# Kernel optimization log

Hardware: AMD Instinct MI355X
Metric: run time of the kernel (lower is better)

The kernel has to match this reference:

```python
import jax, jax.numpy as jnp
import numpy as np

B, N, H, D = 2, 2048, 8, 64  # batch, seq, heads, out_channels (per-head, incl. time dim)
E = H * 64                   # embed dim = num_heads * in_channels
C = 1.0                      # manifold curvature c
EPS = 1e-8


def setup_inputs() -> dict:
    key = jax.random.key(0)
    ks = jax.random.split(key, 8)
    d_out = H * (D - 1)
    inp = {
        "query_input": jax.random.normal(ks[0], (B, N, E), dtype=jnp.float32),
        "source_input": jax.random.normal(ks[1], (B, N, E), dtype=jnp.float32),
        "Wq_w": jax.random.normal(ks[2], (d_out, E), dtype=jnp.float32) * 0.02,
        "Wq_b": jnp.zeros((d_out,), dtype=jnp.float32),
        "Wk_w": jax.random.normal(ks[3], (d_out, E), dtype=jnp.float32) * 0.02,
        "Wk_b": jnp.zeros((d_out,), dtype=jnp.float32),
        "Wv_w": jax.random.normal(ks[4], (d_out, E), dtype=jnp.float32) * 0.02,
        "Wv_b": jnp.zeros((d_out,), dtype=jnp.float32),
        "scale": jnp.array([np.sqrt(H * D)], dtype=jnp.float32),
        "bias": jnp.zeros((), dtype=jnp.float32),
    }
    return inp


def _lift(x_space):
    # project space coords onto hyperboloid: prepend time = sqrt(||x||^2 + c)
    t = jnp.sqrt(jnp.sum(x_space * x_space, axis=-1, keepdims=True) + C)
    return jnp.concatenate([t, x_space], axis=-1)  # [..., D]


def _centroid(ave):
    # Lorentzian centroid normalization: sqrt(c) * ave / sqrt(|<ave,ave>_L|)
    inner = jnp.sum(ave * ave, axis=-1, keepdims=True) - 2.0 * ave[..., :1] ** 2
    denom = jnp.sqrt(jnp.maximum(jnp.abs(inner), EPS))
    return jnp.sqrt(C) * ave / denom


def reference(query_input, source_input, Wq_w, Wq_b, Wk_w, Wk_b, Wv_w, Wv_b, scale, bias):
    def heads(x, W, b):
        return (x @ W.T + b).reshape(B, N, H, D - 1)

    q = _lift(heads(query_input, Wq_w, Wq_b))   # [B,N,H,D]
    k = _lift(heads(source_input, Wk_w, Wk_b))  # [B,N,H,D]
    v = _lift(heads(source_input, Wv_w, Wv_b))  # [B,N,H,D]

    # Lorentzian inner product: negate time component of q
    sign = jnp.concatenate([-jnp.ones((1,), q.dtype), jnp.ones((D - 1,), q.dtype)])
    att = 2.0 * C + 2.0 * jnp.einsum('bnhd,bmhd->bhnm', q * sign, k)  # [B,H,N,N]
    att = att / scale[0] + bias
    w = jax.nn.softmax(att, axis=-1)

    ave = jnp.einsum('bhnm,bmhd->bnhd', w, v)   # weighted sum of values
    out = _centroid(ave)                         # per-head hyperbolic centroid [B,N,H,D]
    out = _centroid(jnp.mean(out, axis=2))       # centroid across heads -> [B,N,D]
    return out
```

## Files before the change

kernel.cpp:

```cpp
#include <hip/hip_runtime.h>
#include <math.h>
#include <stdint.h>

#define BB   2
#define NN   2048
#define HH   8
#define DD   64
#define EE   512
#define DM1  63

typedef _Float16 half8  __attribute__((ext_vector_type(8)));
typedef __fp16   fp16x2 __attribute__((ext_vector_type(2)));
typedef float    floatx4 __attribute__((ext_vector_type(4)));

__device__ __forceinline__ uint32_t pkh2(float a, float b) {
    union { fp16x2 h; uint32_t u; } uu;
    uu.h = __builtin_amdgcn_cvt_pkrtz(a, b);
    return uu.u;
}

__global__ __launch_bounds__(256, 3) void qkv_mfma(
    const float* __restrict__ Xq, const float* __restrict__ Xs,
    const float* __restrict__ Wq, const float* __restrict__ Wk,
    const float* __restrict__ Wv,
    const float* __restrict__ Wqb, const float* __restrict__ Wkb,
    const float* __restrict__ Wvb, const float* __restrict__ scale_p,
    _Float16* __restrict__ q16, _Float16* __restrict__ k16,
    _Float16* __restrict__ vT16)
{
    const int mtb = blockIdx.x;
    const int hp  = blockIdx.y;
    const int mat = blockIdx.z;
    const int t    = threadIdx.x;
    const int w    = t >> 6;
    const int lane = t & 63;
    const int l15  = lane & 15;
    const int quad = lane >> 4;

    __shared__ alignas(16) char smem[27648];
    __shared__ float psum[64][4];
    _Float16 (*Xsh)[72]  = (_Float16(*)[72])smem;
    _Float16 (*Wsh)[72]  = (_Float16(*)[72])(smem + 9216);
    _Float16 (*Osh)[136] = (_Float16(*)[136])(smem + 9216);
    _Float16 (*OshT)[72] = (_Float16(*)[72])(smem + 9216);

    const float* X    = (mat == 0) ? Xq : Xs;
    const float* W    = (mat == 0) ? Wq : (mat == 1 ? Wk : Wv);
    const float* bias = (mat == 0) ? Wqb : (mat == 1 ? Wkb : Wvb);
    const int tok0 = mtb * 64;

    floatx4 acc[4][2];
#pragma unroll
    for (int mt = 0; mt < 4; mt++)
#pragma unroll
        for (int nt = 0; nt < 2; nt++) acc[mt][nt] = (floatx4){0.f,0.f,0.f,0.f};

    float4 pxa[2], pxb[2], pwa[4], pwb[4];
#pragma unroll
    for (int ls = 0; ls < 2; ls++) {
        int g = t + 256 * ls, r = g >> 3, c = g & 7;
        const float* p = X + (size_t)(tok0 + r) * EE + c * 8;
        pxa[ls] = *(const float4*)p;
        pxb[ls] = *(const float4*)(p + 4);
    }
#pragma unroll
    for (int ls = 0; ls < 4; ls++) {
        int g = t + 256 * ls, r = g >> 3, c = g & 7;
        int head = r >> 6, j = r & 63;
        pwa[ls] = make_float4(0.f,0.f,0.f,0.f);
        pwb[ls] = make_float4(0.f,0.f,0.f,0.f);
        if (j < DM1) {
            const float* p = W + (size_t)((hp * 2 + head) * DM1 + j) * EE + c * 8;
            pwa[ls] = *(const float4*)p;
            pwb[ls] = *(const float4*)(p + 4);
        }
    }

    for (int it = 0; it < 8; it++) {
        __syncthreads();
#pragma unroll
        for (int ls = 0; ls < 2; ls++) {
            int g = t + 256 * ls, r = g >> 3, c = g & 7;
            uint4 h;
            h.x = pkh2(pxa[ls].x, pxa[ls].y); h.y = pkh2(pxa[ls].z, pxa[ls].w);
            h.z = pkh2(pxb[ls].x, pxb[ls].y); h.w = pkh2(pxb[ls].z, pxb[ls].w);
            *(uint4*)&Xsh[r][c * 8] = h;
        }
#pragma unroll
        for (int ls = 0; ls < 4; ls++) {
            int g = t + 256 * ls, r = g >> 3, c = g & 7;
            uint4 h;
            h.x = pkh2(pwa[ls].x, pwa[ls].y); h.y = pkh2(pwa[ls].z, pwa[ls].w);
            h.z = pkh2(pwb[ls].x, pwb[ls].y); h.w = pkh2(pwb[ls].z, pwb[ls].w);
            *(uint4*)&Wsh[r][c * 8] = h;
        }
        __syncthreads();
        if (it + 1 < 8) {
            int ek = (it + 1) * 64;
#pragma unroll
            for (int ls = 0; ls < 2; ls++) {
                int g = t + 256 * ls, r = g >> 3, c = g & 7;
                const float* p = X + (size_t)(tok0 + r) * EE + ek + c * 8;
                pxa[ls] = *(const float4*)p;
                pxb[ls] = *(const float4*)(p + 4);
            }
#pragma unroll
            for (int ls = 0; ls < 4; ls++) {
                int g = t + 256 * ls, r = g >> 3, c = g & 7;
                int head = r >> 6, j = r & 63;
                if (j < DM1) {
                    const float* p = W + (size_t)((hp * 2 + head) * DM1 + j) * EE + ek + c * 8;
                    pwa[ls] = *(const float4*)p;
                    pwb[ls] = *(const float4*)(p + 4);
                }
            }
        }
#pragma unroll
        for (int kk = 0; kk < 2; kk++) {
            half8 a[4];
#pragma unroll
            for (int mt = 0; mt < 4; mt++)
                a[mt] = *(const half8*)&Xsh[mt * 16 + l15][kk * 32 + quad * 8];
#pragma unroll
            for (int nt = 0; nt < 2; nt++) {
                half8 bfr = *(const half8*)&Wsh[w * 32 + nt * 16 + l15][kk * 32 + quad * 8];
#pragma unroll
                for (int mt = 0; mt < 4; mt++)
                    acc[mt][nt] = __builtin_amdgcn_mfma_f32_16x16x32_f16(
                        a[mt], bfr, acc[mt][nt], 0, 0, 0);
            }
        }
    }
    __syncthreads();

    const float st   = 2.0f / scale_p[0];
    const float fmul = (mat == 0) ? st : 1.0f;

    float vals[4][2][4];
    float sqp[4][4];
#pragma unroll
    for (int mt = 0; mt < 4; mt++)
#pragma unroll
        for (int r = 0; r < 4; r++) sqp[mt][r] = 0.f;

#pragma unroll
    for (int mt = 0; mt < 4; mt++)
#pragma unroll
        for (int nt = 0; nt < 2; nt++) {
            int col = w * 32 + nt * 16 + l15;
            int head = col >> 6, j = col & 63;
            float bb = (j < DM1) ? bias[(hp * 2 + head) * DM1 + j] : 0.f;
#pragma unroll
            for (int r = 0; r < 4; r++) {
                float vv = acc[mt][nt][r] + bb;
                if (j >= DM1) vv = 0.f;
                vals[mt][nt][r] = vv;
                sqp[mt][r] += vv * vv;
            }
        }
#pragma unroll
    for (int mt = 0; mt < 4; mt++)
#pragma unroll
        for (int r = 0; r < 4; r++) {
            float s = sqp[mt][r];
            s += __shfl_xor(s, 1, 64); s += __shfl_xor(s, 2, 64);
            s += __shfl_xor(s, 4, 64); s += __shfl_xor(s, 8, 64);
            if (l15 == 0) psum[mt * 16 + quad * 4 + r][w] = s;
        }

    if (mat < 2) {
#pragma unroll
        for (int mt = 0; mt < 4; mt++)
#pragma unroll
            for (int nt = 0; nt < 2; nt++) {
                int col = w * 32 + nt * 16 + l15;
                int head = col >> 6, j = col & 63;
                if (j < DM1) {
                    int dc = head * 64 + 1 + j;
#pragma unroll
                    for (int r = 0; r < 4; r++)
                        Osh[mt * 16 + quad * 4 + r][dc] = (_Float16)(vals[mt][nt][r] * fmul);
                }
            }
    } else {
#pragma unroll
        for (int mt = 0; mt < 4; mt++)
#pragma unroll
            for (int nt = 0; nt < 2; nt++) {
                int col = w * 32 + nt * 16 + l15;
                uint2 pu;
                pu.x = pkh2(vals[mt][nt][0], vals[mt][nt][1]);
                pu.y = pkh2(vals[mt][nt][2], vals[mt][nt][3]);
                *(uint2*)&OshT[col][mt * 16 + quad * 4] = pu;
            }
    }
    __syncthreads();
    if (t < 64) {
        float tsA = sqrtf(psum[t][0] + psum[t][1] + 1.0f);
        float tsB = sqrtf(psum[t][2] + psum[t][3] + 1.0f);
        if (mat < 2) {
            float tm = (mat == 0) ? -st : 1.0f;
            Osh[t][0]  = (_Float16)(tsA * tm);
            Osh[t][64] = (_Float16)(tsB * tm);
        } else {
            OshT[63][t]  = (_Float16)tsA;
            OshT[127][t] = (_Float16)tsB;
        }
    }
    __syncthreads();

    const int bI = tok0 >> 11, n0 = tok0 & 2047;
    if (mat < 2) {
        _Float16* O = (mat == 0) ? q16 : k16;
#pragma unroll
        for (int ls = 0; ls < 4; ls++) {
            int s = t + 256 * ls, r = s >> 4, c = s & 15, head = c >> 3;
            size_t bh = (size_t)(bI * HH + hp * 2 + head);
            *(uint4*)&O[(bh * NN + n0 + r) * DD + (c & 7) * 8] = *(const uint4*)&Osh[r][c * 8];
        }
    } else {
#pragma unroll
        for (int ls = 0; ls < 4; ls++) {
            int s = t + 256 * ls, df = s >> 3, c = s & 7;
            int head = df >> 6, d = df & 63;
            int rr = head * 64 + ((d + 63) & 63);
            size_t bh = (size_t)(bI * HH + hp * 2 + head);
            *(uint4*)&vT16[(bh * DD + d) * NN + n0 + c * 8] = *(const uint4*)&OshT[rr][c * 8];
        }
    }
}

__global__ __launch_bounds__(256, 3) void lorentz_attn_v8(
    const _Float16* __restrict__ q16, const _Float16* __restrict__ k16,
    const _Float16* __restrict__ vT16,
    _Float16* __restrict__ Odh, float* __restrict__ Ors)
{
    const int qt = blockIdx.x;
    const int bh = blockIdx.y;
    const int ks = blockIdx.z;
    const int t    = threadIdx.x;
    const int w    = t >> 6;
    const int lane = t & 63;
    const int l15  = lane & 15;
    const int quad = lane >> 4;

    __shared__ alignas(16) char smem[36864];
    _Float16 (*Ks)[72]  = (_Float16(*)[72])smem;
    _Float16 (*VTs)[72] = (_Float16(*)[72])(smem + 9216);
    _Float16 (*Psw)[72] = (_Float16(*)[72])(smem + 18432 + w * 4608);

    const _Float16* kb = k16  + (size_t)bh * NN * DD;
    const _Float16* vb = vT16 + (size_t)bh * DD * NN;
    const int kt0 = ks * 8;

    half8 qb[2][2];
#pragma unroll
    for (int mt = 0; mt < 2; mt++) {
        const _Float16* qrow = q16 +
            ((size_t)bh * NN + qt * 128 + w * 32 + mt * 16 + l15) * DD;
        qb[mt][0] = *(const half8*)&qrow[quad * 8];
        qb[mt][1] = *(const half8*)&qrow[32 + quad * 8];
    }

    half8 vones;
#pragma unroll
    for (int i = 0; i < 8; i++) vones[i] = (_Float16)1.0f;

    uint4 pk[2], pv[2];
#pragma unroll
    for (int ls = 0; ls < 2; ls++) {
        int s = t + 256 * ls, r = s >> 3, c = s & 7;
        pk[ls] = *(const uint4*)&kb[((size_t)kt0 * 64 + r) * DD + c * 8];
        pv[ls] = *(const uint4*)&vb[(size_t)r * NN + kt0 * 64 + c * 8];
    }
#pragma unroll
    for (int ls = 0; ls < 2; ls++) {
        int s = t + 256 * ls, r = s >> 3, c = s & 7;
        *(uint4*)&Ks[r][c * 8]  = pk[ls];
        *(uint4*)&VTs[r][c * 8] = pv[ls];
    }
    __syncthreads();

    floatx4 oacc[2][5];
#pragma unroll
    for (int mt = 0; mt < 2; mt++)
#pragma unroll
        for (int nt = 0; nt < 5; nt++) oacc[mt][nt] = (floatx4){0.f,0.f,0.f,0.f};

    for (int i = 0; i < 8; i++) {
        const int kt = kt0 + i;
        if (i + 1 < 8) {
#pragma unroll
            for (int ls = 0; ls < 2; ls++) {
                int s = t + 256 * ls, r = s >> 3, c = s & 7;
                pk[ls] = *(const uint4*)&kb[((size_t)(kt + 1) * 64 + r) * DD + c * 8];
                pv[ls] = *(const uint4*)&vb[(size_t)r * NN + (kt + 1) * 64 + c * 8];
            }
        }
        floatx4 sacc[4][2];
#pragma unroll
        for (int nt = 0; nt < 4; nt++)
#pragma unroll
            for (int mt = 0; mt < 2; mt++) sacc[nt][mt] = (floatx4){0.f,0.f,0.f,0.f};
#pragma unroll
        for (int kk = 0; kk < 2; kk++)
#pragma unroll
            for (int nt = 0; nt < 4; nt++) {
                half8 kf = *(const half8*)&Ks[nt * 16 + l15][kk * 32 + quad * 8];
#pragma unroll
                for (int mt = 0; mt < 2; mt++)
                    sacc[nt][mt] = __builtin_amdgcn_mfma_f32_16x16x32_f16(
                        kf, qb[mt][kk], sacc[nt][mt], 0, 0, 0);
            }
#pragma unroll
        for (int nt = 0; nt < 4; nt++)
#pragma unroll
            for (int mt = 0; mt < 2; mt++) {
                uint2 pu;
                pu.x = pkh2(__expf(sacc[nt][mt][0]), __expf(sacc[nt][mt][1]));
                pu.y = pkh2(__expf(sacc[nt][mt][2]), __expf(sacc[nt][mt][3]));
                *(uint2*)&Psw[mt * 16 + l15][nt * 16 + quad * 4] = pu;
            }
        half8 pa[2][2];
#pragma unroll
        for (int mt = 0; mt < 2; mt++) {
            pa[mt][0] = *(const half8*)&Psw[mt * 16 + l15][quad * 8];
            pa[mt][1] = *(const half8*)&Psw[mt * 16 + l15][32 + quad * 8];
        }
#pragma unroll
        for (int kk = 0; kk < 2; kk++) {
#pragma unroll
            for (int nt = 0; nt < 4; nt++) {
                half8 vf = *(const half8*)&VTs[nt * 16 + l15][kk * 32 + quad * 8];
#pragma unroll
                for (int mt = 0; mt < 2; mt++)
                    oacc[mt][nt] = __builtin_amdgcn_mfma_f32_16x16x32_f16(
                        pa[mt][kk], vf, oacc[mt][nt], 0, 0, 0);
            }
#pragma unroll
            for (int mt = 0; mt < 2; mt++)
                oacc[mt][4] = __builtin_amdgcn_mfma_f32_16x16x32_f16(
                    pa[mt][kk], vones, oacc[mt][4], 0, 0, 0);
        }
        __syncthreads();
        if (i + 1 < 8) {
#pragma unroll
            for (int ls = 0; ls < 2; ls++) {
                int s = t + 256 * ls, r = s >> 3, c = s & 7;
                *(uint4*)&Ks[r][c * 8]  = pk[ls];
                *(uint4*)&VTs[r][c * 8] = pv[ls];
            }
            __syncthreads();
        }
    }

    const size_t obase = (((size_t)ks * 16 + bh) * NN + qt * 128 + w * 32);
    float* slab = (float*)Psw;
#pragma unroll
    for (int mt = 0; mt < 2; mt++) {
#pragma unroll
        for (int nt = 0; nt < 4; nt++)
#pragma unroll
            for (int r = 0; r < 4; r++)
                slab[(quad * 4 + r) * 68 + nt * 16 + l15] = oacc[mt][nt][r];
#pragma unroll
        for (int i = 0; i < 4; i++) {
            int s = lane + 64 * i, row = s >> 4, c4 = (s & 15) * 4;
            float4 v = *(const float4*)&slab[row * 68 + c4];
            uint2 pu;
            pu.x = pkh2(v.x, v.y);
            pu.y = pkh2(v.z, v.w);
            *(uint2*)&Odh[(obase + mt * 16 + row) * 64 + c4] = pu;
        }
        if (l15 == 0) {
#pragma unroll
            for (int r = 0; r < 4; r++)
                Ors[obase + mt * 16 + quad * 4 + r] = oacc[mt][4][r];
        }
    }
}

__global__ __launch_bounds__(256) void merge_centroid(
    const _Float16* __restrict__ Odh, const float* __restrict__ Ors,
    float* __restrict__ out)
{
    const int t    = threadIdx.x;
    const int tok  = blockIdx.x * 4 + (t >> 6);
    const int lane = t & 63;
    const int b = tok >> 11;
    const int n = tok & 2047;

    float m = 0.f;
#pragma unroll
    for (int h = 0; h < HH; h++) {
        const size_t bh = (size_t)(b * HH + h);
        float o = 0.f, rs = 0.f;
#pragma unroll
        for (int ksp = 0; ksp < 4; ksp++) {
            const size_t row = ((size_t)ksp * 16 + bh) * NN + n;
            o  += (float)Odh[row * 64 + lane];
            rs += Ors[row];
        }
        float a  = o / rs;
        float ssq = a * a;
#pragma unroll
        for (int off = 32; off > 0; off >>= 1)
            ssq += __shfl_xor(ssq, off, 64);
        float a0 = __shfl(a, 0, 64);
        float inner = ssq - 2.0f * a0 * a0;
        float f = rsqrtf(fmaxf(fabsf(inner), 1e-8f));
        m += a * f;
    }
    m *= 0.125f;

    float sq = m * m;
#pragma unroll
    for (int off = 32; off > 0; off >>= 1)
        sq += __shfl_xor(sq, off, 64);
    float m0 = __shfl(m, 0, 64);
    float inner = sq - 2.0f * m0 * m0;
    float f = rsqrtf(fmaxf(fabsf(inner), 1e-8f));
    out[(size_t)tok * DD + lane] = m * f;
}

extern "C" void kernel_launch(void* const* d_in, const int* in_sizes, int n_in,
                              void* d_out, int out_size, void* d_ws, size_t ws_size,
                              hipStream_t stream)
{
    const float* Xq  = (const float*)d_in[0];
    const float* Xs  = (const float*)d_in[1];
    const float* Wq  = (const float*)d_in[2];
    const float* Wqb = (const float*)d_in[3];
    const float* Wk  = (const float*)d_in[4];
    const float* Wkb = (const float*)d_in[5];
    const float* Wv  = (const float*)d_in[6];
    const float* Wvb = (const float*)d_in[7];
    const float* sc  = (const float*)d_in[8];
    float* out = (float*)d_out;

    const size_t QSZ = (size_t)BB * HH * NN * DD;
    _Float16* q16  = (_Float16*)d_ws;
    _Float16* k16  = q16 + QSZ;
    _Float16* vT16 = k16 + QSZ;
    _Float16* Odh  = vT16 + QSZ;
    float* Ors = (float*)(Odh + (size_t)4 * 16 * NN * 64);

    qkv_mfma<<<dim3(64, 4, 3), 256, 0, stream>>>(Xq, Xs, Wq, Wk, Wv,
                                                 Wqb, Wkb, Wvb, sc,
                                                 q16, k16, vT16);
    lorentz_attn_v8<<<dim3(16, 16, 4), 256, 0, stream>>>(q16, k16, vT16, Odh, Ors);
    merge_centroid<<<(BB * NN) / 4, 256, 0, stream>>>(Odh, Ors, out);
}
```

Baseline: 150.9 us.

## Double query tile per block and double-buffer K/V shared tiles

Each attention block now handles 256 query rows (64 per wave) instead of 128, so every K/V tile staged in shared memory is reused across twice as many queries. K/V shared buffers become double-buffered, which leaves one __syncthreads per iteration instead of two. The S computation is restructured per key subtile to limit live accumulators. In exchange, shared memory doubles to 72KB, register pressure rises (20 output accumulators per lane), launch bounds drop to 2 blocks per CU, and the grid halves to 512 blocks.

```diff
diff --git a/kernel.cpp b/kernel.cpp
--- a/kernel.cpp
+++ b/kernel.cpp
@@ -230,7 +230,7 @@
     }
 }
 
-__global__ __launch_bounds__(256, 3) void lorentz_attn_v8(
+__global__ __launch_bounds__(256, 2) void lorentz_attn_v9(
     const _Float16* __restrict__ q16, const _Float16* __restrict__ k16,
     const _Float16* __restrict__ vT16,
     _Float16* __restrict__ Odh, float* __restrict__ Ors)
@@ -244,20 +244,18 @@
     const int l15  = lane & 15;
     const int quad = lane >> 4;
 
-    __shared__ alignas(16) char smem[36864];
-    _Float16 (*Ks)[72]  = (_Float16(*)[72])smem;
-    _Float16 (*VTs)[72] = (_Float16(*)[72])(smem + 9216);
-    _Float16 (*Psw)[72] = (_Float16(*)[72])(smem + 18432 + w * 4608);
+    __shared__ alignas(16) char smem[73728];
+    _Float16 (*Psw)[72] = (_Float16(*)[72])(smem + 36864 + w * 9216);
 
     const _Float16* kb = k16  + (size_t)bh * NN * DD;
     const _Float16* vb = vT16 + (size_t)bh * DD * NN;
     const int kt0 = ks * 8;
 
-    half8 qb[2][2];
-#pragma unroll
-    for (int mt = 0; mt < 2; mt++) {
+    half8 qb[4][2];
+#pragma unroll
+    for (int mt = 0; mt < 4; mt++) {
         const _Float16* qrow = q16 +
-            ((size_t)bh * NN + qt * 128 + w * 32 + mt * 16 + l15) * DD;
+            ((size_t)bh * NN + qt * 256 + w * 64 + mt * 16 + l15) * DD;
         qb[mt][0] = *(const half8*)&qrow[quad * 8];
         qb[mt][1] = *(const half8*)&qrow[32 + quad * 8];
     }
@@ -276,19 +274,23 @@
 #pragma unroll
     for (int ls = 0; ls < 2; ls++) {
         int s = t + 256 * ls, r = s >> 3, c = s & 7;
-        *(uint4*)&Ks[r][c * 8]  = pk[ls];
-        *(uint4*)&VTs[r][c * 8] = pv[ls];
+        *(uint4*)(smem +         (size_t)r * 144 + c * 16) = pk[ls];
+        *(uint4*)(smem + 18432 + (size_t)r * 144 + c * 16) = pv[ls];
     }
     __syncthreads();
 
-    floatx4 oacc[2][5];
-#pragma unroll
-    for (int mt = 0; mt < 2; mt++)
+    floatx4 oacc[4][5];
+#pragma unroll
+    for (int mt = 0; mt < 4; mt++)
 #pragma unroll
         for (int nt = 0; nt < 5; nt++) oacc[mt][nt] = (floatx4){0.f,0.f,0.f,0.f};
 
     for (int i = 0; i < 8; i++) {
         const int kt = kt0 + i;
+        const int buf = i & 1;
+        _Float16 (*Ks)[72]  = (_Float16(*)[72])(smem + buf * 9216);
+        _Float16 (*VTs)[72] = (_Float16(*)[72])(smem + 18432 + buf * 9216);
+
         if (i + 1 < 8) {
 #pragma unroll
             for (int ls = 0; ls < 2; ls++) {
@@ -297,67 +299,66 @@
                 pv[ls] = *(const uint4*)&vb[(size_t)r * NN + (kt + 1) * 64 + c * 8];
             }
         }
-        floatx4 sacc[4][2];
-#pragma unroll
-        for (int nt = 0; nt < 4; nt++)
-#pragma unroll
-            for (int mt = 0; mt < 2; mt++) sacc[nt][mt] = (floatx4){0.f,0.f,0.f,0.f};
-#pragma unroll
-        for (int kk = 0; kk < 2; kk++)
-#pragma unroll
-            for (int nt = 0; nt < 4; nt++) {
+
+#pragma unroll
+        for (int nt = 0; nt < 4; nt++) {
+            floatx4 sacc[4];
+#pragma unroll
+            for (int mt = 0; mt < 4; mt++) sacc[mt] = (floatx4){0.f,0.f,0.f,0.f};
+#pragma unroll
+            for (int kk = 0; kk < 2; kk++) {
                 half8 kf = *(const half8*)&Ks[nt * 16 + l15][kk * 32 + quad * 8];
 #pragma unroll
-                for (int mt = 0; mt < 2; mt++)
-                    sacc[nt][mt] = __builtin_amdgcn_mfma_f32_16x16x32_f16(
-                        kf, qb[mt][kk], sacc[nt][mt], 0, 0, 0);
-            }
-#pragma unroll
-        for (int nt = 0; nt < 4; nt++)
-#pragma unroll
-            for (int mt = 0; mt < 2; mt++) {
+                for (int mt = 0; mt < 4; mt++)
+                    sacc[mt] = __builtin_amdgcn_mfma_f32_16x16x32_f16(
+                        kf, qb[mt][kk], sacc[mt], 0, 0, 0);
+            }
+#pragma unroll
+            for (int mt = 0; mt < 4; mt++) {
                 uint2 pu;
-                pu.x = pkh2(__expf(sacc[nt][mt][0]), __expf(sacc[nt][mt][1]));
-                pu.y = pkh2(__expf(sacc[nt][mt][2]), __expf(sacc[nt][mt][3]));
+                pu.x = pkh2(__expf(sacc[mt][0]), __expf(sacc[mt][1]));
+                pu.y = pkh2(__expf(sacc[mt][2]), __expf(sacc[mt][3]));
                 *(uint2*)&Psw[mt * 16 + l15][nt * 16 + quad * 4] = pu;
             }
-        half8 pa[2][2];
-#pragma unroll
-        for (int mt = 0; mt < 2; mt++) {
-            pa[mt][0] = *(const half8*)&Psw[mt * 16 + l15][quad * 8];
-            pa[mt][1] = *(const half8*)&Psw[mt * 16 + l15][32 + quad * 8];
-        }
+        }
+
 #pragma unroll
         for (int kk = 0; kk < 2; kk++) {
+            half8 pa[4];
+#pragma unroll
+            for (int mt = 0; mt < 4; mt++)
+                pa[mt] = *(const half8*)&Psw[mt * 16 + l15][kk * 32 + quad * 8];
 #pragma unroll
             for (int nt = 0; nt < 4; nt++) {
                 half8 vf = *(const half8*)&VTs[nt * 16 + l15][kk * 32 + quad * 8];
 #pragma unroll
-                for (int mt = 0; mt < 2; mt++)
+                for (int mt = 0; mt < 4; mt++)
                     oacc[mt][nt] = __builtin_amdgcn_mfma_f32_16x16x32_f16(
-                        pa[mt][kk], vf, oacc[mt][nt], 0, 0, 0);
-            }
-#pragma unroll
-            for (int mt = 0; mt < 2; mt++)
+                        pa[mt], vf, oacc[mt][nt], 0, 0, 0);
+            }
+#pragma unroll
+            for (int mt = 0; mt < 4; mt++)
                 oacc[mt][4] = __builtin_amdgcn_mfma_f32_16x16x32_f16(
-                    pa[mt][kk], vones, oacc[mt][4], 0, 0, 0);
-        }
-        __syncthreads();
+                    pa[mt], vones, oacc[mt][4], 0, 0, 0);
+        }
+
         if (i + 1 < 8) {
+            char* kd = smem +         (1 - buf) * 9216;
+            char* vd = smem + 18432 + (1 - buf) * 9216;
 #pragma unroll
             for (int ls = 0; ls < 2; ls++) {
                 int s = t + 256 * ls, r = s >> 3, c = s & 7;
-                *(uint4*)&Ks[r][c * 8]  = pk[ls];
-                *(uint4*)&VTs[r][c * 8] = pv[ls];
-            }
-            __syncthreads();
-        }
-    }
-
-    const size_t obase = (((size_t)ks * 16 + bh) * NN + qt * 128 + w * 32);
+                *(uint4*)(kd + (size_t)r * 144 + c * 16) = pk[ls];
+                *(uint4*)(vd + (size_t)r * 144 + c * 16) = pv[ls];
+            }
+        }
+        __syncthreads();
+    }
+
+    const size_t obase = (((size_t)ks * 16 + bh) * NN + qt * 256 + w * 64);
     float* slab = (float*)Psw;
 #pragma unroll
-    for (int mt = 0; mt < 2; mt++) {
+    for (int mt = 0; mt < 4; mt++) {
 #pragma unroll
         for (int nt = 0; nt < 4; nt++)
 #pragma unroll
@@ -448,6 +449,6 @@
     qkv_mfma<<<dim3(64, 4, 3), 256, 0, stream>>>(Xq, Xs, Wq, Wk, Wv,
                                                  Wqb, Wkb, Wvb, sc,
                                                  q16, k16, vT16);
-    lorentz_attn_v8<<<dim3(16, 16, 4), 256, 0, stream>>>(q16, k16, vT16, Odh, Ors);
+    lorentz_attn_v9<<<dim3(8, 16, 4), 256, 0, stream>>>(q16, k16, vT16, Odh, Ors);
     merge_centroid<<<(BB * NN) / 4, 256, 0, stream>>>(Odh, Ors, out);
 }
```

Measured after the change: 129.7 us. 1.16x faster.
